# Performance work log

Measured on AMD Instinct MI355X. Metric: run time of the kernel, lower is better.

Reference implementation:

```python
import jax, jax.numpy as jnp
import numpy as np

N_SPECIES = 8192
N_RXN = 16384
N_UNBAL = 512
N_BAL = N_SPECIES - N_UNBAL
STOICH_DENSITY = 0.002  # ~16 participating species per reaction


def setup_inputs() -> dict:
    key = jax.random.key(0)
    k0, k1, k2, k3, k4 = jax.random.split(key, 5)
    # positive balanced concentrations in (0.1, 1.1)
    conc_balanced = jax.random.uniform(k0, (N_BAL,), jnp.float32, 0.1, 1.1)
    # sparse integer-valued stoichiometric matrix S[s, r]
    vals = jax.random.randint(k1, (N_SPECIES, N_RXN), -2, 3).astype(jnp.float32)
    mask = jax.random.bernoulli(k2, STOICH_DENSITY, (N_SPECIES, N_RXN))
    S = vals * mask
    balanced_species = jnp.arange(N_BAL, dtype=jnp.int32)
    unbalanced_species = jnp.arange(N_BAL, N_SPECIES, dtype=jnp.int32)
    log_conc_unbalanced = jax.random.normal(k3, (N_UNBAL,), jnp.float32) * 0.1
    log_kcat = jax.random.normal(k4, (N_RXN,), jnp.float32) * 0.1
    return {
        "conc_balanced": conc_balanced,
        "S": S,
        "balanced_species": balanced_species,
        "unbalanced_species": unbalanced_species,
        "log_conc_unbalanced": log_conc_unbalanced,
        "log_kcat": log_kcat,
    }


def reference(conc_balanced, S, balanced_species, unbalanced_species,
              log_conc_unbalanced, log_kcat):
    # --- KineticModel.flux ---
    # scatter balanced and (exp of log) unbalanced concentrations into full vector
    conc = jnp.zeros(S.shape[0], dtype=conc_balanced.dtype)
    conc = conc.at[balanced_species].set(conc_balanced)
    conc = conc.at[unbalanced_species].set(jnp.exp(log_conc_unbalanced))
    # vectorized per-reaction mass-action rate law:
    # v_r = kcat_r * prod_s conc_s ** max(-S[s,r], 0)
    sub_stoich = jnp.maximum(-S, 0.0)              # substrate stoichiometry [s, r]
    log_v = log_kcat + sub_stoich.T @ jnp.log(conc)  # [r]
    v = jnp.exp(log_v)
    # --- KineticModel.dcdt ---
    dcdt = (S @ v)[balanced_species]               # [n_balanced]
    return dcdt
```

## Files before the change

### kernel.cpp

```cpp
#include <hip/hip_runtime.h>
#include <math.h>

#define NSPEC 8192
#define NRXN  16384
#define NBAL  7680
#define NUNBAL 512

#define NBLOCK 2048
#define NTHREAD 256
#define NWAVE ((NBLOCK * NTHREAD) / 64)
#define SLOTS 64

#define OFF_LOGC  0u
#define OFF_LOGV  32768u
#define OFF_ACC   98304u
#define OFF_CNT   131072u
#define OFF_WCNT  131088u
#define OFF_SLICE (OFF_WCNT + NWAVE * 4u)
#define OFF_SPILL (OFF_SLICE + NWAVE * SLOTS * 4u)


__global__ void k_init(const float* __restrict__ cb, const int* __restrict__ bidx,
                       const int* __restrict__ uidx, const float* __restrict__ lcu,
                       const float* __restrict__ lkcat,
                       float* __restrict__ logc, float* __restrict__ logv,
                       float* __restrict__ acc, unsigned* __restrict__ cnt) {
    int i = blockIdx.x * blockDim.x + threadIdx.x;
    if (i == 0) *cnt = 0u;
    if (i < NRXN)  logv[i] = lkcat[i];
    if (i < NSPEC) acc[i] = 0.0f;
    if (i < NBAL)  logc[bidx[i]] = logf(cb[i]);
    if (i < NUNBAL) logc[uidx[i]] = lcu[i];
}

__global__ __launch_bounds__(256) void k_scan(const float* __restrict__ S,
                                              const float* __restrict__ logc,
                                              float* __restrict__ logv,
                                              unsigned* __restrict__ wcnt,
                                              unsigned* __restrict__ slices,
                                              unsigned* __restrict__ spillcnt,
                                              unsigned* __restrict__ spill,
                                              unsigned spillcap) {
    const int lane = threadIdx.x & 63;
    const unsigned gid = blockIdx.x * blockDim.x + threadIdx.x;
    const unsigned wave = gid >> 6;
    unsigned* const slice = slices + (size_t)wave * SLOTS;
    unsigned base = 0;
    const long long nvec = (long long)NSPEC * (long long)NRXN / 4;
    const long long stride = (long long)gridDim.x * blockDim.x;
    for (long long i = gid; i < nvec; i += stride) {
        const float4 f = ((const float4*)S)[i];
        bool any = (f.x != 0.0f) | (f.y != 0.0f) | (f.z != 0.0f) | (f.w != 0.0f);
        if (__ballot(any) == 0ULL) continue;
        const float vals[4] = {f.x, f.y, f.z, f.w};
        const int s = (int)(i >> 12);
        const int rbase = ((int)i & 4095) << 2;
        #pragma unroll
        for (int j = 0; j < 4; ++j) {
            float val = vals[j];
            bool nz = (val != 0.0f);
            unsigned long long m = __ballot(nz);
            if (m == 0ULL) continue;
            if (nz) {
                int r = rbase + j;
                int iv = (int)val;
                if (val < 0.0f)
                    atomicAdd(&logv[r], (float)(-iv) * logc[s]);
                unsigned pos = base +
                    (unsigned)__popcll(m & ((1ULL << lane) - 1ULL));
                unsigned e = ((unsigned)s << 17) | ((unsigned)r << 3) |
                             (unsigned)(iv + 2);
                if (pos < SLOTS) {
                    slice[pos] = e;
                } else {
                    unsigned sp = atomicAdd(spillcnt, 1u);
                    if (sp < spillcap) spill[sp] = e;
                }
            }
            base += (unsigned)__popcll(m);
        }
    }
    if (lane == 0) wcnt[wave] = (base < SLOTS) ? base : SLOTS;
}

__global__ void k_exp(float* __restrict__ logv) {
    int i = blockIdx.x * blockDim.x + threadIdx.x;
    if (i < NRXN) logv[i] = expf(logv[i]);
}

__global__ __launch_bounds__(256) void k_scatter(const unsigned* __restrict__ slices,
                                                 const unsigned* __restrict__ wcnt,
                                                 const unsigned* __restrict__ spill,
                                                 const unsigned* __restrict__ spillcnt,
                                                 unsigned spillcap,
                                                 const float* __restrict__ v,
                                                 float* __restrict__ acc) {
    unsigned idx = blockIdx.x * blockDim.x + threadIdx.x;
    if (idx < (unsigned)NWAVE * SLOTS) {
        unsigned wave = idx >> 6, slot = idx & 63u;
        if (slot < wcnt[wave]) {
            unsigned e = slices[idx];
            int s = (int)(e >> 17);
            int r = (int)((e >> 3) & 0x3FFFu);
            float iv = (float)((int)(e & 7u) - 2);
            atomicAdd(&acc[s], iv * v[r]);
        }
    }
    unsigned n = *spillcnt;
    if (n > spillcap) n = spillcap;
    unsigned stride = gridDim.x * blockDim.x;
    for (unsigned i = idx; i < n; i += stride) {
        unsigned e = spill[i];
        int s = (int)(e >> 17);
        int r = (int)((e >> 3) & 0x3FFFu);
        float iv = (float)((int)(e & 7u) - 2);
        atomicAdd(&acc[s], iv * v[r]);
    }
}

__global__ __launch_bounds__(256) void k_scan_noent(const float* __restrict__ S,
                                                    const float* __restrict__ logc,
                                                    float* __restrict__ logv) {
    const long long nvec = (long long)NSPEC * (long long)NRXN / 4;
    const long long stride = (long long)gridDim.x * blockDim.x;
    for (long long i = (long long)blockIdx.x * blockDim.x + threadIdx.x;
         i < nvec; i += stride) {
        const float4 f = ((const float4*)S)[i];
        const float vals[4] = {f.x, f.y, f.z, f.w};
        if (f.x < 0.0f || f.y < 0.0f || f.z < 0.0f || f.w < 0.0f) {
            int s = (int)(i >> 12);
            int rbase = ((int)i & 4095) << 2;
            #pragma unroll
            for (int j = 0; j < 4; ++j)
                if (vals[j] < 0.0f)
                    atomicAdd(&logv[rbase + j], -vals[j] * logc[s]);
        }
    }
}

__global__ __launch_bounds__(256) void k_pass2(const float* __restrict__ S,
                                               const float* __restrict__ v,
                                               float* __restrict__ acc) {
    const long long nvec = (long long)NSPEC * (long long)NRXN / 4;
    const long long stride = (long long)gridDim.x * blockDim.x;
    for (long long i = (long long)blockIdx.x * blockDim.x + threadIdx.x;
         i < nvec; i += stride) {
        const float4 f = ((const float4*)S)[i];
        const float vals[4] = {f.x, f.y, f.z, f.w};
        if (f.x != 0.0f || f.y != 0.0f || f.z != 0.0f || f.w != 0.0f) {
            int s = (int)(i >> 12);
            int rbase = ((int)i & 4095) << 2;
            #pragma unroll
            for (int j = 0; j < 4; ++j)
                if (vals[j] != 0.0f)
                    atomicAdd(&acc[s], vals[j] * v[rbase + j]);
        }
    }
}

__global__ void k_gather(const float* __restrict__ acc,
                         const int* __restrict__ bidx,
                         float* __restrict__ out) {
    int i = blockIdx.x * blockDim.x + threadIdx.x;
    if (i < NBAL) out[i] = acc[bidx[i]];
}

extern "C" void kernel_launch(void* const* d_in, const int* in_sizes, int n_in,
                              void* d_out, int out_size, void* d_ws, size_t ws_size,
                              hipStream_t stream) {
    const float* cb    = (const float*)d_in[0];
    const float* S     = (const float*)d_in[1];
    const int*   bidx  = (const int*)d_in[2];
    const int*   uidx  = (const int*)d_in[3];
    const float* lcu   = (const float*)d_in[4];
    const float* lkcat = (const float*)d_in[5];
    float* out = (float*)d_out;

    char* ws = (char*)d_ws;
    float*    logc    = (float*)(ws + OFF_LOGC);
    float*    logv    = (float*)(ws + OFF_LOGV);
    float*    acc     = (float*)(ws + OFF_ACC);
    unsigned* cnt     = (unsigned*)(ws + OFF_CNT);
    unsigned* wcnt    = (unsigned*)(ws + OFF_WCNT);
    unsigned* slices  = (unsigned*)(ws + OFF_SLICE);
    unsigned* spill   = (unsigned*)(ws + OFF_SPILL);

    k_init<<<(NRXN + 255) / 256, 256, 0, stream>>>(cb, bidx, uidx, lcu, lkcat,
                                                   logc, logv, acc, cnt);
    if (ws_size >= OFF_SPILL + 65536u) {
        unsigned spillcap = (unsigned)((ws_size - OFF_SPILL) / 4);
        k_scan<<<NBLOCK, NTHREAD, 0, stream>>>(S, logc, logv, wcnt, slices,
                                               cnt, spill, spillcap);
        k_exp<<<(NRXN + 255) / 256, 256, 0, stream>>>(logv);
        k_scatter<<<NBLOCK, NTHREAD, 0, stream>>>(slices, wcnt, spill, cnt,
                                                  spillcap, logv, acc);
    } else {
        k_scan_noent<<<NBLOCK, NTHREAD, 0, stream>>>(S, logc, logv);
        k_exp<<<(NRXN + 255) / 256, 256, 0, stream>>>(logv);
        k_pass2<<<NBLOCK, NTHREAD, 0, stream>>>(S, logv, acc);
    }
    k_gather<<<(NBAL + 255) / 256, 256, 0, stream>>>(acc, bidx, out);
}
```

Measured before the change: 712.9 us.

## Restructure stoichiometry scan into wave chunks with per-thread entry slices, fuse exp

The scan kernel now has each wave walk contiguous 256-int4 chunks, issuing four independent loads per iteration, and drops the per-element ballot/popcount compaction in favour of per-thread 8-slot entry buffers. The separate exp kernel is removed and the exponential is computed inline when scattering. The scatter launch is sized to the new slot layout. The aim is more memory-level parallelism and fewer wave-wide ops on the 512 MB streaming read. In exchange, exp is recomputed once per nonzero entry, and threads that fill their slots spill through a global atomic counter.

```diff
diff --git a/kernel.cpp b/kernel.cpp
--- a/kernel.cpp
+++ b/kernel.cpp
@@ -6,18 +6,23 @@
 #define NBAL  7680
 #define NUNBAL 512
 
-#define NBLOCK 2048
+#define NBLOCK  2048
 #define NTHREAD 256
-#define NWAVE ((NBLOCK * NTHREAD) / 64)
-#define SLOTS 64
+#define NTHREADS_TOTAL (NBLOCK * NTHREAD)
+#define NWAVES_TOTAL   (NTHREADS_TOTAL / 64)
+#define TSLOTS 8
+
+#define NVEC4  ((long long)NSPEC * NRXN / 4)
+#define CHUNK  256
+#define NCHUNK (NVEC4 / CHUNK)
 
 #define OFF_LOGC  0u
 #define OFF_LOGV  32768u
 #define OFF_ACC   98304u
 #define OFF_CNT   131072u
-#define OFF_WCNT  131088u
-#define OFF_SLICE (OFF_WCNT + NWAVE * 4u)
-#define OFF_SPILL (OFF_SLICE + NWAVE * SLOTS * 4u)
+#define OFF_TCNT  131088u
+#define OFF_SLICE (OFF_TCNT + NTHREADS_TOTAL * 4u)
+#define OFF_SPILL (OFF_SLICE + NTHREADS_TOTAL * TSLOTS * 4u)
 
 
 __global__ void k_init(const float* __restrict__ cb, const int* __restrict__ bidx,
@@ -33,77 +38,83 @@
     if (i < NUNBAL) logc[uidx[i]] = lcu[i];
 }
 
+__device__ __forceinline__ void proc_group(int4 g, long long idx,
+                                           const float* __restrict__ logc,
+                                           float* __restrict__ logv,
+                                           unsigned* __restrict__ slice,
+                                           unsigned& lc,
+                                           unsigned* __restrict__ spillcnt,
+                                           unsigned* __restrict__ spill,
+                                           unsigned spillcap) {
+    if ((g.x | g.y | g.z | g.w) == 0) return;
+    const int s = (int)(idx >> 12);
+    const int rbase = ((int)idx & 4095) << 2;
+    const float lcs = logc[s];
+    const int vb[4] = {g.x, g.y, g.z, g.w};
+    #pragma unroll
+    for (int j = 0; j < 4; ++j) {
+        if (vb[j] != 0) {
+            float val = __int_as_float(vb[j]);
+            int iv = (int)val;
+            if (val < 0.0f)
+                atomicAdd(&logv[rbase + j], -val * lcs);
+            unsigned e = ((unsigned)s << 17) | ((unsigned)(rbase + j) << 3) |
+                         (unsigned)(iv + 2);
+            if (lc < TSLOTS) {
+                slice[lc] = e;
+            } else {
+                unsigned sp = atomicAdd(spillcnt, 1u);
+                if (sp < spillcap) spill[sp] = e;
+            }
+            lc++;
+        }
+    }
+}
+
 __global__ __launch_bounds__(256) void k_scan(const float* __restrict__ S,
                                               const float* __restrict__ logc,
                                               float* __restrict__ logv,
-                                              unsigned* __restrict__ wcnt,
+                                              unsigned* __restrict__ tcnt,
                                               unsigned* __restrict__ slices,
                                               unsigned* __restrict__ spillcnt,
                                               unsigned* __restrict__ spill,
                                               unsigned spillcap) {
+    const unsigned tid = blockIdx.x * blockDim.x + threadIdx.x;
+    const unsigned wid = tid >> 6;
     const int lane = threadIdx.x & 63;
-    const unsigned gid = blockIdx.x * blockDim.x + threadIdx.x;
-    const unsigned wave = gid >> 6;
-    unsigned* const slice = slices + (size_t)wave * SLOTS;
-    unsigned base = 0;
-    const long long nvec = (long long)NSPEC * (long long)NRXN / 4;
-    const long long stride = (long long)gridDim.x * blockDim.x;
-    for (long long i = gid; i < nvec; i += stride) {
-        const float4 f = ((const float4*)S)[i];
-        bool any = (f.x != 0.0f) | (f.y != 0.0f) | (f.z != 0.0f) | (f.w != 0.0f);
-        if (__ballot(any) == 0ULL) continue;
-        const float vals[4] = {f.x, f.y, f.z, f.w};
-        const int s = (int)(i >> 12);
-        const int rbase = ((int)i & 4095) << 2;
-        #pragma unroll
-        for (int j = 0; j < 4; ++j) {
-            float val = vals[j];
-            bool nz = (val != 0.0f);
-            unsigned long long m = __ballot(nz);
-            if (m == 0ULL) continue;
-            if (nz) {
-                int r = rbase + j;
-                int iv = (int)val;
-                if (val < 0.0f)
-                    atomicAdd(&logv[r], (float)(-iv) * logc[s]);
-                unsigned pos = base +
-                    (unsigned)__popcll(m & ((1ULL << lane) - 1ULL));
-                unsigned e = ((unsigned)s << 17) | ((unsigned)r << 3) |
-                             (unsigned)(iv + 2);
-                if (pos < SLOTS) {
-                    slice[pos] = e;
-                } else {
-                    unsigned sp = atomicAdd(spillcnt, 1u);
-                    if (sp < spillcap) spill[sp] = e;
-                }
-            }
-            base += (unsigned)__popcll(m);
-        }
-    }
-    if (lane == 0) wcnt[wave] = (base < SLOTS) ? base : SLOTS;
-}
-
-__global__ void k_exp(float* __restrict__ logv) {
-    int i = blockIdx.x * blockDim.x + threadIdx.x;
-    if (i < NRXN) logv[i] = expf(logv[i]);
+    const int4* S4 = (const int4*)S;
+    unsigned* const slice = slices + (size_t)tid * TSLOTS;
+    unsigned lc = 0;
+    for (long long c = wid; c < NCHUNK; c += NWAVES_TOTAL) {
+        const long long b = c * CHUNK + lane;
+        int4 g0 = S4[b];
+        int4 g1 = S4[b + 64];
+        int4 g2 = S4[b + 128];
+        int4 g3 = S4[b + 192];
+        proc_group(g0, b,       logc, logv, slice, lc, spillcnt, spill, spillcap);
+        proc_group(g1, b + 64,  logc, logv, slice, lc, spillcnt, spill, spillcap);
+        proc_group(g2, b + 128, logc, logv, slice, lc, spillcnt, spill, spillcap);
+        proc_group(g3, b + 192, logc, logv, slice, lc, spillcnt, spill, spillcap);
+    }
+    tcnt[tid] = (lc < TSLOTS) ? lc : TSLOTS;
 }
 
 __global__ __launch_bounds__(256) void k_scatter(const unsigned* __restrict__ slices,
-                                                 const unsigned* __restrict__ wcnt,
+                                                 const unsigned* __restrict__ tcnt,
                                                  const unsigned* __restrict__ spill,
                                                  const unsigned* __restrict__ spillcnt,
                                                  unsigned spillcap,
-                                                 const float* __restrict__ v,
+                                                 const float* __restrict__ logv,
                                                  float* __restrict__ acc) {
     unsigned idx = blockIdx.x * blockDim.x + threadIdx.x;
-    if (idx < (unsigned)NWAVE * SLOTS) {
-        unsigned wave = idx >> 6, slot = idx & 63u;
-        if (slot < wcnt[wave]) {
+    if (idx < (unsigned)NTHREADS_TOTAL * TSLOTS) {
+        unsigned t = idx >> 3, slot = idx & 7u;
+        if (slot < tcnt[t]) {
             unsigned e = slices[idx];
             int s = (int)(e >> 17);
             int r = (int)((e >> 3) & 0x3FFFu);
             float iv = (float)((int)(e & 7u) - 2);
-            atomicAdd(&acc[s], iv * v[r]);
+            atomicAdd(&acc[s], iv * expf(logv[r]));
         }
     }
     unsigned n = *spillcnt;
@@ -114,17 +125,16 @@
         int s = (int)(e >> 17);
         int r = (int)((e >> 3) & 0x3FFFu);
         float iv = (float)((int)(e & 7u) - 2);
-        atomicAdd(&acc[s], iv * v[r]);
+        atomicAdd(&acc[s], iv * expf(logv[r]));
     }
 }
 
 __global__ __launch_bounds__(256) void k_scan_noent(const float* __restrict__ S,
                                                     const float* __restrict__ logc,
                                                     float* __restrict__ logv) {
-    const long long nvec = (long long)NSPEC * (long long)NRXN / 4;
     const long long stride = (long long)gridDim.x * blockDim.x;
     for (long long i = (long long)blockIdx.x * blockDim.x + threadIdx.x;
-         i < nvec; i += stride) {
+         i < NVEC4; i += stride) {
         const float4 f = ((const float4*)S)[i];
         const float vals[4] = {f.x, f.y, f.z, f.w};
         if (f.x < 0.0f || f.y < 0.0f || f.z < 0.0f || f.w < 0.0f) {
@@ -139,12 +149,11 @@
 }
 
 __global__ __launch_bounds__(256) void k_pass2(const float* __restrict__ S,
-                                               const float* __restrict__ v,
+                                               const float* __restrict__ logv,
                                                float* __restrict__ acc) {
-    const long long nvec = (long long)NSPEC * (long long)NRXN / 4;
     const long long stride = (long long)gridDim.x * blockDim.x;
     for (long long i = (long long)blockIdx.x * blockDim.x + threadIdx.x;
-         i < nvec; i += stride) {
+         i < NVEC4; i += stride) {
         const float4 f = ((const float4*)S)[i];
         const float vals[4] = {f.x, f.y, f.z, f.w};
         if (f.x != 0.0f || f.y != 0.0f || f.z != 0.0f || f.w != 0.0f) {
@@ -153,7 +162,7 @@
             #pragma unroll
             for (int j = 0; j < 4; ++j)
                 if (vals[j] != 0.0f)
-                    atomicAdd(&acc[s], vals[j] * v[rbase + j]);
+                    atomicAdd(&acc[s], vals[j] * expf(logv[rbase + j]));
         }
     }
 }
@@ -177,26 +186,24 @@
     float* out = (float*)d_out;
 
     char* ws = (char*)d_ws;
-    float*    logc    = (float*)(ws + OFF_LOGC);
-    float*    logv    = (float*)(ws + OFF_LOGV);
-    float*    acc     = (float*)(ws + OFF_ACC);
-    unsigned* cnt     = (unsigned*)(ws + OFF_CNT);
-    unsigned* wcnt    = (unsigned*)(ws + OFF_WCNT);
-    unsigned* slices  = (unsigned*)(ws + OFF_SLICE);
-    unsigned* spill   = (unsigned*)(ws + OFF_SPILL);
+    float*    logc   = (float*)(ws + OFF_LOGC);
+    float*    logv   = (float*)(ws + OFF_LOGV);
+    float*    acc    = (float*)(ws + OFF_ACC);
+    unsigned* cnt    = (unsigned*)(ws + OFF_CNT);
+    unsigned* tcnt   = (unsigned*)(ws + OFF_TCNT);
+    unsigned* slices = (unsigned*)(ws + OFF_SLICE);
+    unsigned* spill  = (unsigned*)(ws + OFF_SPILL);
 
     k_init<<<(NRXN + 255) / 256, 256, 0, stream>>>(cb, bidx, uidx, lcu, lkcat,
                                                    logc, logv, acc, cnt);
     if (ws_size >= OFF_SPILL + 65536u) {
         unsigned spillcap = (unsigned)((ws_size - OFF_SPILL) / 4);
-        k_scan<<<NBLOCK, NTHREAD, 0, stream>>>(S, logc, logv, wcnt, slices,
+        k_scan<<<NBLOCK, NTHREAD, 0, stream>>>(S, logc, logv, tcnt, slices,
                                                cnt, spill, spillcap);
-        k_exp<<<(NRXN + 255) / 256, 256, 0, stream>>>(logv);
-        k_scatter<<<NBLOCK, NTHREAD, 0, stream>>>(slices, wcnt, spill, cnt,
-                                                  spillcap, logv, acc);
+        k_scatter<<<(NTHREADS_TOTAL * TSLOTS) / 256, 256, 0, stream>>>(
+            slices, tcnt, spill, cnt, spillcap, logv, acc);
     } else {
         k_scan_noent<<<NBLOCK, NTHREAD, 0, stream>>>(S, logc, logv);
-        k_exp<<<(NRXN + 255) / 256, 256, 0, stream>>>(logv);
         k_pass2<<<NBLOCK, NTHREAD, 0, stream>>>(S, logv, acc);
     }
     k_gather<<<(NBAL + 255) / 256, 256, 0, stream>>>(acc, bidx, out);
```

New measurement: 760.0 us. 6.6% more time.
